# Optimization experiments

Measured on AMD Instinct MI355X. Metric: run time of the kernel, lower is better.

## Reference

```python
import jax, jax.numpy as jnp
import numpy as np

_PADE_B = np.array([6.476475253248e+16, 3.238237626624e+16, 7771770303897600.0,
                    1187353796428800.0, 129060195264000.0, 10559470521600.0,
                    670442572800.0, 33522128640.0, 1323241920.0, 40840800.0,
                    960960.0, 16380.0, 182.0, 1.0])
_MAXNORM = 5.371920351148152
_MAX_SQUARINGS = 6  # randn 3x3 has Fro norm ~3 < maxnorm; 6 steps is ample headroom


def _expm(A):
    """Batched scaling-and-squaring Pade-13 matrix exponential. A: [N, d, d]."""
    b = _PADE_B.astype(A.dtype)
    d = A.shape[-1]
    ident = jnp.eye(d, dtype=A.dtype)
    fro = jnp.sqrt(jnp.sum(A * A, axis=(1, 2), keepdims=True))  # [N,1,1]
    n_sq = jnp.maximum(0.0, jnp.ceil(jnp.log2(fro / _MAXNORM)))
    Ascaled = A / (2.0 ** n_sq)
    n_sq_i = n_sq.reshape(-1).astype(jnp.int32)  # [N]

    A2 = Ascaled @ Ascaled
    A4 = A2 @ A2
    A6 = A4 @ A2
    U = Ascaled @ (A6 @ (b[13] * A6 + b[11] * A4 + b[9] * A2)
                   + b[7] * A6 + b[5] * A4 + b[3] * A2 + b[1] * ident)
    V = (A6 @ (b[12] * A6 + b[10] * A4 + b[8] * A2)
         + b[6] * A6 + b[4] * A4 + b[2] * A2 + b[0] * ident)
    P = U + V
    Q = -U + V
    R = jnp.linalg.solve(Q, P)  # torch.solve(P, Q): Q X = P

    def body(k, R):
        R2 = R @ R
        return jnp.where((k < n_sq_i)[:, None, None], R2, R)

    return jax.lax.fori_loop(0, _MAX_SQUARINGS, body, R, unroll=True)


def setup_inputs() -> dict:
    key = jax.random.key(0)
    k1, k2, k3 = jax.random.split(key, 3)
    bs, n, d = 65536, 24, 3
    return {
        "mean": jax.random.normal(k1, (bs, n, d), dtype=jnp.float32),
        "var": jax.random.normal(k2, (bs, n, d, d), dtype=jnp.float32),
        "gt": jax.random.normal(k3, (bs, n, d), dtype=jnp.float32),
    }


def reference(mean, var, gt):
    bs, n, d = mean.shape
    A = var.reshape(bs * n, d, d)
    E = _expm(A)                               # [bs*n, d, d]
    delta = (gt - mean).reshape(bs * n, d)     # [bs*n, d]
    quad = jnp.einsum('ni,nij,nj->n', delta, E, delta)
    dets = jnp.linalg.det(A)
    per = 0.5 * (quad + dets) / n              # [bs*n]
    loss = per.reshape(bs, n).sum(axis=1)      # [bs]
    return loss.mean()
```

## Files before the change

kernel.cpp:

```cpp
#include <hip/hip_runtime.h>

#define TPB 256

#define B0c  6.476475253248e+16f
#define B1c  3.238237626624e+16f
#define B2c  7.7717703038976e+15f
#define B3c  1.1873537964288e+15f
#define B4c  1.29060195264e+14f
#define B5c  1.05594705216e+13f
#define B6c  6.704425728e+11f
#define B7c  3.352212864e+10f
#define B8c  1.32324192e+9f
#define B9c  4.08408e+7f
#define B10c 9.6096e+5f
#define B11c 1.638e+4f
#define B12c 182.0f
#define B13c 1.0f

__device__ __forceinline__ float expm_loss_one(
    float a0, float a1, float a2, float a3, float a4, float a5,
    float a6, float a7, float a8, float d0, float d1, float d2) {
  const float detA = a0 * (a4 * a8 - a5 * a7)
                   - a1 * (a3 * a8 - a5 * a6)
                   + a2 * (a3 * a7 - a4 * a6);
  const float trA = a0 + a4 + a8;
  const float trA2 = fmaf(a0, a0, fmaf(a4, a4, a8 * a8))
                   + 2.0f * (fmaf(a1, a3, fmaf(a2, a6, a5 * a7)));
  float fro2 = fmaf(a0, a0, fmaf(a1, a1, a2 * a2));
  fro2 = fmaf(a3, a3, fmaf(a4, a4, fmaf(a5, a5, fro2)));
  fro2 = fmaf(a6, a6, fmaf(a7, a7, fmaf(a8, a8, fro2)));
  const float u0 = fmaf(a0, d0, fmaf(a1, d1, a2 * d2));
  const float u1 = fmaf(a3, d0, fmaf(a4, d1, a5 * d2));
  const float u2 = fmaf(a6, d0, fmaf(a7, d1, a8 * d2));
  const float v0 = fmaf(a0, d0, fmaf(a3, d1, a6 * d2));
  const float v1 = fmaf(a1, d0, fmaf(a4, d1, a7 * d2));
  const float v2 = fmaf(a2, d0, fmaf(a5, d1, a8 * d2));
  const float dAd  = fmaf(d0, u0, fmaf(d1, u1, d2 * u2));
  const float dA2d = fmaf(v0, u0, fmaf(v1, u1, v2 * u2));
  const float dd   = fmaf(d0, d0, fmaf(d1, d1, d2 * d2));

  const float nsqf = fmaxf(0.0f, ceilf(fmaf(0.5f, __log2f(fro2), -2.4253625f)));
  int nsq = (int)nsqf;
  nsq = nsq > 6 ? 6 : nsq;
  const float scl = exp2f(-nsqf);
  const float scl2 = scl * scl;

  const float t = scl * trA;
  const float trB2 = scl2 * trA2;
  const float m = 0.5f * fmaf(t, t, -trB2);
  const float dch = detA * scl2 * scl;

  const float x4p = fmaf(t, t, -m), x4q = fmaf(-t, m, dch), x4r = t * dch;
  const float x5p = fmaf(x4p, t, x4q), x5q = fmaf(-x4p, m, x4r), x5r = x4p * dch;
  const float x6p = fmaf(x5p, t, x5q), x6q = fmaf(-x5p, m, x5r), x6r = x5p * dch;

  const float w1p = fmaf(B11c, x4p, x6p) + B9c;
  const float w1q = fmaf(B11c, x4q, x6q);
  const float w1r = fmaf(B11c, x4r, x6r);
  const float s4a = x6p * w1p;
  const float s3a = fmaf(x6p, w1q, x6q * w1p);
  const float gp = fmaf(s4a, x4p, fmaf(s3a, t,   fmaf(x6p, w1r, fmaf(x6r, w1p, x6q * w1q))));
  const float gq = fmaf(s4a, x4q, fmaf(-s3a, m,  fmaf(x6q, w1r, x6r * w1q)));
  const float gr = fmaf(s4a, x4r, fmaf(s3a, dch, x6r * w1r));
  const float uep = fmaf(B7c, x6p, fmaf(B5c, x4p, gp)) + B3c;
  const float ueq = fmaf(B7c, x6q, fmaf(B5c, x4q, gq));
  const float uer = fmaf(B7c, x6r, fmaf(B5c, x4r, gr)) + B1c;
  const float up = fmaf(uep, t, ueq);
  const float uq = fmaf(-uep, m, uer);
  const float ur = uep * dch;

  const float w2p = fmaf(B12c, x6p, fmaf(B10c, x4p, B8c));
  const float w2q = fmaf(B12c, x6q, B10c * x4q);
  const float w2r = fmaf(B12c, x6r, B10c * x4r);
  const float s4b = x6p * w2p;
  const float s3b = fmaf(x6p, w2q, x6q * w2p);
  const float hp = fmaf(s4b, x4p, fmaf(s3b, t,   fmaf(x6p, w2r, fmaf(x6r, w2p, x6q * w2q))));
  const float hq = fmaf(s4b, x4q, fmaf(-s3b, m,  fmaf(x6q, w2r, x6r * w2q)));
  const float hr = fmaf(s4b, x4r, fmaf(s3b, dch, x6r * w2r));
  const float vp = fmaf(B6c, x6p, fmaf(B4c, x4p, hp)) + B2c;
  const float vq = fmaf(B6c, x6q, fmaf(B4c, x4q, hq));
  const float vr = fmaf(B6c, x6r, fmaf(B4c, x4r, hr)) + B0c;

  const float s = 1.0f / B0c;
  const float pp = (vp + up) * s, pq = (vq + uq) * s, pr = (vr + ur) * s;
  const float qp = (vp - up) * s, qq = (vq - uq) * s, qr = (vr - ur) * s;

  const float qpp = qp * qp, qpq2 = 2.0f * qp * qq;
  const float a2t = fmaf(qpp, x4p, fmaf(qpq2, t,   fmaf(2.0f * qp, qr, qq * qq)));
  const float b2t = fmaf(qpp, x4q, fmaf(-qpq2, m,  2.0f * qq * qr));
  const float c2t = fmaf(qpp, x4r, fmaf(qpq2, dch, qr * qr));
  const float tQ = fmaf(qp, trB2, fmaf(qq, t, 3.0f * qr));
  const float trQ2 = fmaf(a2t, trB2, fmaf(b2t, t, 3.0f * c2t));
  const float mQ = 0.5f * fmaf(tQ, tQ, -trQ2);
  const float detQ =
      qp * (fmaf(qp, fmaf(qp, dch * dch, fmaf(qq, m * dch, qr * fmaf(m, m, -2.0f * t * dch))),
                 fmaf(qq, fmaf(qq, t * dch, qr * fmaf(t, m, -3.0f * dch)),
                      qr * qr * fmaf(t, t, -2.0f * m))))
    + qq * fmaf(qq, fmaf(qq, dch, qr * m), qr * qr * t)
    + qr * qr * qr;
  float inv = __builtin_amdgcn_rcpf(detQ);
  inv = inv * (2.0f - detQ * inv);
  const float jp = fmaf(-tQ, qp, a2t);
  const float jq = fmaf(-tQ, qq, b2t);
  const float jr = fmaf(-tQ, qr, c2t) + mQ;

  const float s4 = pp * jp;
  const float s3 = fmaf(pp, jq, pq * jp);
  float rp = fmaf(s4, x4p, fmaf(s3, t,   fmaf(pp, jr, fmaf(pr, jp, pq * jq)))) * inv;
  float rq = fmaf(s4, x4q, fmaf(-s3, m,  fmaf(pq, jr, pr * jq))) * inv;
  float rr = fmaf(s4, x4r, fmaf(s3, dch, pr * jr)) * inv;

  for (int k = 0; k < nsq; ++k) {
    const float rp2 = rp * rp, rpq2 = 2.0f * rp * rq;
    const float nrp = fmaf(rp2, x4p, fmaf(rpq2, t,   fmaf(2.0f * rp, rr, rq * rq)));
    const float nrq = fmaf(rp2, x4q, fmaf(-rpq2, m,  2.0f * rq * rr));
    const float nrr = fmaf(rp2, x4r, fmaf(rpq2, dch, rr * rr));
    rp = nrp; rq = nrq; rr = nrr;
  }

  const float quad = fmaf(rp, scl2 * dA2d, fmaf(rq, scl * dAd, rr * dd));
  return 0.5f * (quad + detA);
}

__global__ __launch_bounds__(TPB) void expm_loss_kernel(
    const float* __restrict__ mean, const float* __restrict__ var,
    const float* __restrict__ gt, float* __restrict__ partials) {
  __shared__ float sA[TPB * 9];
  __shared__ float sD[TPB * 3];
  const int tid = threadIdx.x;
  const long long base = (long long)blockIdx.x * TPB;

  const float4* v4 = (const float4*)(var + base * 9);
  float4* sA4 = (float4*)sA;
  sA4[tid]       = v4[tid];
  sA4[tid + 256] = v4[tid + 256];
  if (tid < 64) sA4[tid + 512] = v4[tid + 512];
  if (tid < 192) {
    const float4 mw = ((const float4*)(mean + base * 3))[tid];
    const float4 gw = ((const float4*)(gt + base * 3))[tid];
    ((float4*)sD)[tid] = make_float4(gw.x - mw.x, gw.y - mw.y,
                                     gw.z - mw.z, gw.w - mw.w);
  }
  __syncthreads();

  const float* a = sA + tid * 9;
  const float* dp = sD + tid * 3;
  float val = expm_loss_one(a[0], a[1], a[2], a[3], a[4], a[5], a[6], a[7], a[8],
                            dp[0], dp[1], dp[2]);

#pragma unroll
  for (int offx = 32; offx > 0; offx >>= 1) val += __shfl_down(val, offx, 64);
  __shared__ float wsum[TPB / 64];
  if ((tid & 63) == 0) wsum[tid >> 6] = val;
  __syncthreads();
  if (tid == 0) {
    float b = 0.f;
#pragma unroll
    for (int wi = 0; wi < TPB / 64; ++wi) b += wsum[wi];
    partials[blockIdx.x] = b;
  }
}

#define RTPB 1024
__global__ __launch_bounds__(RTPB) void reduce_partials_kernel(
    const float* __restrict__ partials, int n, double inv_total,
    float* __restrict__ out) {
  double s = 0.0;
  for (int i = threadIdx.x; i < n; i += RTPB) s += (double)partials[i];
#pragma unroll
  for (int off = 32; off > 0; off >>= 1) s += __shfl_down(s, off, 64);
  __shared__ double ds[RTPB / 64];
  if ((threadIdx.x & 63) == 0) ds[threadIdx.x >> 6] = s;
  __syncthreads();
  if (threadIdx.x == 0) {
    double b = 0.0;
#pragma unroll
    for (int w = 0; w < RTPB / 64; ++w) b += ds[w];
    out[0] = (float)(b * inv_total);
  }
}

extern "C" void kernel_launch(void* const* d_in, const int* in_sizes, int n_in,
                              void* d_out, int out_size, void* d_ws, size_t ws_size,
                              hipStream_t stream) {
  const float* mean = (const float*)d_in[0];
  const float* var  = (const float*)d_in[1];
  const float* gt   = (const float*)d_in[2];
  const int nmat    = in_sizes[1] / 9;
  const int nblocks = nmat / TPB;
  float* partials   = (float*)d_ws;

  expm_loss_kernel<<<nblocks, TPB, 0, stream>>>(mean, var, gt, partials);
  reduce_partials_kernel<<<1, RTPB, 0, stream>>>(partials, nblocks,
                                                 1.0 / (double)nmat,
                                                 (float*)d_out);
}
```

Before: 24.99 us.

## Process three tiles per block with double-buffered LDS staging

Each block now handles three 256-matrix tiles instead of one, using two LDS buffers so the global loads for the next tile are issued before computing the current one. This aims to overlap memory latency with the expm arithmetic and to cut block count and partial-sum work. It doubles LDS use per block, which may lower occupancy, and it assumes the matrix count is divisible by 768 (1572864/768=2048, so this holds for the test size).

```diff
diff --git a/kernel.cpp b/kernel.cpp
--- a/kernel.cpp
+++ b/kernel.cpp
@@ -1,6 +1,7 @@
 #include <hip/hip_runtime.h>
 
 #define TPB 256
+#define TILES 3
 
 #define B0c  6.476475253248e+16f
 #define B1c  3.238237626624e+16f
@@ -122,31 +123,49 @@
   return 0.5f * (quad + detA);
 }
 
+__device__ __forceinline__ void stage_tile(
+    const float* __restrict__ mean, const float* __restrict__ var,
+    const float* __restrict__ gt, long long tile, int tid,
+    float* dA, float* dD) {
+  const long long mbase = tile * TPB;
+  const float4* v4 = (const float4*)(var + mbase * 9);
+  float4* a4 = (float4*)dA;
+  a4[tid]       = v4[tid];
+  a4[tid + 256] = v4[tid + 256];
+  if (tid < 64) a4[tid + 512] = v4[tid + 512];
+  if (tid < 192) {
+    const float4 mw = ((const float4*)(mean + mbase * 3))[tid];
+    const float4 gw = ((const float4*)(gt + mbase * 3))[tid];
+    ((float4*)dD)[tid] = make_float4(gw.x - mw.x, gw.y - mw.y,
+                                     gw.z - mw.z, gw.w - mw.w);
+  }
+}
+
+__device__ __forceinline__ float compute_tile(const float* bA, const float* bD,
+                                              int tid) {
+  const float* a = bA + tid * 9;
+  const float* dp = bD + tid * 3;
+  return expm_loss_one(a[0], a[1], a[2], a[3], a[4], a[5], a[6], a[7], a[8],
+                       dp[0], dp[1], dp[2]);
+}
+
 __global__ __launch_bounds__(TPB) void expm_loss_kernel(
     const float* __restrict__ mean, const float* __restrict__ var,
     const float* __restrict__ gt, float* __restrict__ partials) {
-  __shared__ float sA[TPB * 9];
-  __shared__ float sD[TPB * 3];
+  __shared__ float sA[2][TPB * 9];
+  __shared__ float sD[2][TPB * 3];
   const int tid = threadIdx.x;
-  const long long base = (long long)blockIdx.x * TPB;
-
-  const float4* v4 = (const float4*)(var + base * 9);
-  float4* sA4 = (float4*)sA;
-  sA4[tid]       = v4[tid];
-  sA4[tid + 256] = v4[tid + 256];
-  if (tid < 64) sA4[tid + 512] = v4[tid + 512];
-  if (tid < 192) {
-    const float4 mw = ((const float4*)(mean + base * 3))[tid];
-    const float4 gw = ((const float4*)(gt + base * 3))[tid];
-    ((float4*)sD)[tid] = make_float4(gw.x - mw.x, gw.y - mw.y,
-                                     gw.z - mw.z, gw.w - mw.w);
-  }
-  __syncthreads();
-
-  const float* a = sA + tid * 9;
-  const float* dp = sD + tid * 3;
-  float val = expm_loss_one(a[0], a[1], a[2], a[3], a[4], a[5], a[6], a[7], a[8],
-                            dp[0], dp[1], dp[2]);
+  const long long tile0 = (long long)blockIdx.x * TILES;
+
+  stage_tile(mean, var, gt, tile0, tid, sA[0], sD[0]);
+  __syncthreads();
+  stage_tile(mean, var, gt, tile0 + 1, tid, sA[1], sD[1]);
+  float val = compute_tile(sA[0], sD[0], tid);
+  __syncthreads();
+  stage_tile(mean, var, gt, tile0 + 2, tid, sA[0], sD[0]);
+  val += compute_tile(sA[1], sD[1], tid);
+  __syncthreads();
+  val += compute_tile(sA[0], sD[0], tid);
 
 #pragma unroll
   for (int offx = 32; offx > 0; offx >>= 1) val += __shfl_down(val, offx, 64);
@@ -187,7 +206,7 @@
   const float* var  = (const float*)d_in[1];
   const float* gt   = (const float*)d_in[2];
   const int nmat    = in_sizes[1] / 9;
-  const int nblocks = nmat / TPB;
+  const int nblocks = nmat / (TPB * TILES);
   float* partials   = (float*)d_ws;
 
   expm_loss_kernel<<<nblocks, TPB, 0, stream>>>(mean, var, gt, partials);
```

After: 26.39 us. +5.6%, slower.
